# Kernel tuning notes

Measured on AMD Instinct MI355X. Metric: run time of the kernel, lower is better.

The kernel has to match this reference:

```python
import jax, jax.numpy as jnp
import numpy as np

B, S, D, H, FF = 2, 2048, 1024, 16, 4096
DK = D // H
MAX_SEQ_LEN = 2048
THETA = 10000.0
EPS = 1e-5


def _linear_init(key, out_f, in_f):
    std = (2.0 / (in_f + out_f)) ** 0.5
    return std * jax.random.truncated_normal(key, -3.0, 3.0, (out_f, in_f), dtype=jnp.float32)


def setup_inputs() -> dict:
    key = jax.random.key(0)
    ks = jax.random.split(key, 9)
    x = jax.random.normal(ks[0], (B, S, D), dtype=jnp.float32)
    token_positions = jnp.broadcast_to(jnp.arange(S, dtype=jnp.int32)[None, :], (B, S))
    return {
        "x": x,
        "wq": _linear_init(ks[1], D, D),
        "wk": _linear_init(ks[2], D, D),
        "wv": _linear_init(ks[3], D, D),
        "wo": _linear_init(ks[4], D, D),
        "w1": _linear_init(ks[5], FF, D),
        "w2": _linear_init(ks[6], D, FF),
        "w3": _linear_init(ks[7], FF, D),
        "g1": jnp.ones((D,), dtype=jnp.float32),
        "g2": jnp.ones((D,), dtype=jnp.float32),
        "token_positions": token_positions,
    }


def _rmsnorm(x, g):
    x32 = x.astype(jnp.float32)
    ms = jnp.sqrt(jnp.mean(x32 * x32, axis=-1, keepdims=True) + EPS)
    return ((x32 / ms) * g).astype(x.dtype)


def _rope(x, pos):
    # x: (B, H, S, DK); pos: (B, S)
    inv_freq = 1.0 / THETA ** (jnp.arange(0, DK, 2, dtype=jnp.float32) / DK)  # (DK/2,)
    freqs = pos.astype(jnp.float32)[..., None] * inv_freq  # (B, S, DK/2)
    cos = jnp.cos(freqs)[:, None, :, :]  # (B, 1, S, DK/2) broadcast over heads
    sin = jnp.sin(freqs)[:, None, :, :]
    x_real = x[..., 0::2]
    x_imag = x[..., 1::2]
    rot_real = x_real * cos - x_imag * sin
    rot_imag = x_real * sin + x_imag * cos
    return jnp.stack([rot_real, rot_imag], axis=-1).reshape(x.shape)


def reference(x, wq, wk, wv, wo, w1, w2, w3, g1, g2, token_positions):
    # --- attention sublayer ---
    h = _rmsnorm(x, g1)
    def proj(w):
        y = jnp.einsum('bsd,ed->bse', h, w)
        return y.reshape(B, S, H, DK).transpose(0, 2, 1, 3)  # (B,H,S,DK)
    Q = _rope(proj(wq), token_positions)
    K = _rope(proj(wk), token_positions)
    V = proj(wv)
    scores = jnp.einsum('bhqd,bhkd->bhqk', Q, K)  # (B,H,S,S) full matrix (naive)
    causal = jnp.tril(jnp.ones((S, S), dtype=bool))
    scores = jnp.where(causal, scores, -jnp.inf) / (DK ** 0.5)
    probs = jax.nn.softmax(scores, axis=-1)
    attn = jnp.einsum('bhqk,bhkd->bhqd', probs, V)
    attn = attn.transpose(0, 2, 1, 3).reshape(B, S, D)
    attn = jnp.einsum('bsd,ed->bse', attn, wo)
    y = x + attn
    # --- SwiGLU FFN sublayer ---
    h2 = _rmsnorm(y, g2)
    a = jnp.einsum('bsd,fd->bsf', h2, w1)
    gate = jnp.einsum('bsd,fd->bsf', h2, w3)
    ff = jnp.einsum('bsf,df->bsd', a * jax.nn.sigmoid(a) * gate, w2)
    return y + ff
```

## Files before the change

kernel.cpp:

```cpp
#include <hip/hip_runtime.h>
#include <hip/hip_bf16.h>

#define B_ 2
#define S_ 2048
#define D_ 1024
#define H_ 16
#define DK_ 64
#define FF_ 4096
#define M_ (B_ * S_)

typedef unsigned short u16;
typedef __bf16 bf16x8 __attribute__((ext_vector_type(8)));
typedef float f32x4 __attribute__((ext_vector_type(4)));
typedef u16 u16x4 __attribute__((ext_vector_type(4)));
typedef u16 u16x8 __attribute__((ext_vector_type(8)));

__device__ __forceinline__ u16 f2bf(float f) {
  __bf16 b = (__bf16)f;
  return __builtin_bit_cast(u16, b);
}
__device__ __forceinline__ float bf2f(u16 u) {
  __bf16 b = __builtin_bit_cast(__bf16, u);
  return (float)b;
}

__device__ __forceinline__ void async_lds16(const void* g, void* l) {
  __builtin_amdgcn_global_load_lds(
      (const __attribute__((address_space(1))) unsigned int*)g,
      (__attribute__((address_space(3))) unsigned int*)l, 16, 0, 0);
}

__device__ __forceinline__ void raw_barrier() {
  asm volatile("s_barrier" ::: "memory");
}
#define VMCNT_WAIT(n) asm volatile("s_waitcnt vmcnt(" #n ")" ::: "memory")

__global__ __launch_bounds__(256) void f2b_all(
    const float* __restrict__ wq, const float* __restrict__ wk,
    const float* __restrict__ wv, const float* __restrict__ wo,
    const float* __restrict__ w1, const float* __restrict__ w2,
    const float* __restrict__ w3, u16* __restrict__ wqkvb,
    u16* __restrict__ wob, u16* __restrict__ wb13, u16* __restrict__ w2b) {
  int i4 = blockIdx.x * 256 + threadIdx.x;
  const float* src;
  u16* dst;
  int off, oo;
  if (i4 < 262144) { src = wq; dst = wqkvb; off = i4; oo = off; }
  else if (i4 < 524288) { src = wk; dst = wqkvb + 1048576; off = i4 - 262144; oo = off; }
  else if (i4 < 786432) { src = wv; dst = wqkvb + 2097152; off = i4 - 524288; oo = off; }
  else if (i4 < 1048576) { src = wo; dst = wob; off = i4 - 786432; oo = off; }
  else if (i4 < 2097152) {
    src = w1; dst = wb13; off = i4 - 1048576;
    const int r = off >> 8;
    oo = (((r >> 4) * 32) + (r & 15)) * 256 + (off & 255);
  } else if (i4 < 3145728) { src = w2; dst = w2b; off = i4 - 2097152; oo = off; }
  else {
    src = w3; dst = wb13; off = i4 - 3145728;
    const int r = off >> 8;
    oo = (((r >> 4) * 32) + 16 + (r & 15)) * 256 + (off & 255);
  }
  float4 v = ((const float4*)src)[off];
  u16x4 o;
  o[0] = f2bf(v.x); o[1] = f2bf(v.y); o[2] = f2bf(v.z); o[3] = f2bf(v.w);
  *(u16x4*)(dst + (size_t)oo * 4) = o;
}

__global__ __launch_bounds__(256) void rmsnorm_k(const float* __restrict__ X,
                                                 const float* __restrict__ G,
                                                 u16* __restrict__ Out) {
  const int row = blockIdx.x, tid = threadIdx.x;
  const float4 xv = *(const float4*)(X + (size_t)row * D_ + tid * 4);
  float ss = xv.x * xv.x + xv.y * xv.y + xv.z * xv.z + xv.w * xv.w;
#pragma unroll
  for (int off = 1; off < 64; off <<= 1) ss += __shfl_xor(ss, off);
  __shared__ float red[4];
  if ((tid & 63) == 0) red[tid >> 6] = ss;
  __syncthreads();
  const float tot = red[0] + red[1] + red[2] + red[3];
  const float sc = rsqrtf(tot * (1.0f / D_) + 1e-5f);
  const float4 gv = *(const float4*)(G + tid * 4);
  u16x4 o;
  o[0] = f2bf(xv.x * sc * gv.x);
  o[1] = f2bf(xv.y * sc * gv.y);
  o[2] = f2bf(xv.z * sc * gv.z);
  o[3] = f2bf(xv.w * sc * gv.w);
  *(u16x4*)(Out + (size_t)row * D_ + tid * 4) = o;
}

__global__ __launch_bounds__(256) void rope2_k(unsigned int* __restrict__ Qb,
                                               unsigned int* __restrict__ Kb,
                                               const int* __restrict__ pos) {
  int idx = blockIdx.x * 256 + threadIdx.x;
  unsigned int* buf = Qb;
  float scale = 0.125f;
  if (idx >= 2097152) { buf = Kb; scale = 1.f; idx -= 2097152; }
  const int row = idx >> 9, p = idx & 511;
  const int i = p & 31;
  unsigned int v = buf[(size_t)row * 512 + p];
  const float xr = bf2f((u16)(v & 0xffffu));
  const float xi = bf2f((u16)(v >> 16));
  const float ang =
      (float)pos[row] * __expf(-(float)i * (9.210340371976184f / 32.0f));
  float sn, cs;
  sincosf(ang, &sn, &cs);
  const float orr = (xr * cs - xi * sn) * scale;
  const float oii = (xr * sn + xi * cs) * scale;
  buf[(size_t)row * 512 + p] =
      (unsigned int)f2bf(orr) | ((unsigned int)f2bf(oii) << 16);
}

__global__ __launch_bounds__(256) void transpose_v(const u16* __restrict__ V,
                                                   u16* __restrict__ Vt) {
  __shared__ __align__(16) u16 tile[32][64];
  const int tid = threadIdx.x;
  const int s0 = blockIdx.x * 32, bh = blockIdx.y, b = bh >> 4, h = bh & 15;
  {
    const int sr = tid >> 3, c = tid & 7;
    *(u16x8*)&tile[sr][c * 8] =
        *(const u16x8*)(V + (size_t)(b * S_ + s0 + sr) * D_ + h * DK_ + c * 8);
  }
  __syncthreads();
  {
    const int dk = tid >> 2, cs = tid & 3;
    u16x8 vv;
#pragma unroll
    for (int j = 0; j < 8; ++j) vv[j] = tile[cs * 8 + j][dk];
    *(u16x8*)(Vt + (size_t)(bh * DK_ + dk) * S_ + s0 + cs * 8) = vv;
  }
}

template <int RGN, int RGM>
__device__ __forceinline__ void region_map(int id, int gx, int BM, int BN,
                                           int& m0, int& n0) {
  const int xcd = id & 7, j = id >> 3;
  const int rcols = gx / RGN;
  m0 = ((xcd / rcols) * RGM + j / RGN) * BM;
  n0 = ((xcd % rcols) * RGN + (j % RGN)) * BN;
}

template <int EPI, int BN, int RGN, int RGM>
__global__ __launch_bounds__(512) void gemm8ph(const u16* __restrict__ A,
                                               const u16* __restrict__ Bw,
                                               void* __restrict__ Cout,
                                               const void* __restrict__ auxp,
                                               int N, int K) {
  constexpr int BM = 256, BK = 64;
  constexpr int CPR = BK / 8;
  constexpr int ACH = BM * CPR;
  constexpr int TCH = (BM + BN) * CPR;
  constexpr int NL = TCH / 512;
  constexpr int NR = BN / 64;
  __shared__ __align__(16) u16 As[2][BM * BK];
  __shared__ __align__(16) u16 Bs[2][BN * BK];
  const int tid = threadIdx.x, l = tid & 63, w = tid >> 6;
  const int gx = gridDim.x;
  const int id = blockIdx.y * gx + blockIdx.x;
  int m0, n0;
  region_map<RGN, RGM>(id, gx, BM, BN, m0, n0);
  const int wm = (w >> 2) * 128, wn = (w & 3) * (BN / 4);
  const int lr = l & 15, lg = l >> 4;

  f32x4 acc[8][NR] = {};

  auto STAGE_ALL = [&](int bf, int k0) {
#pragma unroll
    for (int i = 0; i < NL; ++i) {
      const int s = i * 512 + tid;
      const int base = i * 512 + w * 64;
      if (base < ACH) {
        const int r = s / CPR, ch = s % CPR;
        async_lds16(A + (size_t)(m0 + r) * K + k0 + ((ch ^ (r & 7)) * 8),
                    (char*)As[bf] + base * 16);
      } else {
        const int s2 = s - ACH;
        const int r = s2 / CPR, ch = s2 % CPR;
        async_lds16(Bw + (size_t)(n0 + r) * K + k0 + ((ch ^ (r & 7)) * 8),
                    (char*)Bs[bf] + (base - ACH) * 16);
      }
    }
  };

  STAGE_ALL(0, 0);
  VMCNT_WAIT(0);
  raw_barrier();
  int cur = 0;
  for (int k0 = 0; k0 < K; k0 += BK) {
    const bool more = (k0 + BK) < K;
    bf16x8 bfr[NR];
#pragma unroll
    for (int ph = 0; ph < 4; ++ph) {
      const int kk = ph >> 1, iq = ph & 1;
      if (iq == 0) {
#pragma unroll
        for (int j = 0; j < NR; ++j) {
          const int row = wn + j * 16 + lr;
          bfr[j] = *(const bf16x8*)&Bs[cur][row * BK +
                                            (((kk * 4 + lg) ^ (row & 7)) * 8)];
        }
      }
      bf16x8 af[4];
#pragma unroll
      for (int i = 0; i < 4; ++i) {
        const int row = wm + (iq * 4 + i) * 16 + lr;
        af[i] = *(const bf16x8*)&As[cur][row * BK +
                                         (((kk * 4 + lg) ^ (row & 7)) * 8)];
      }
      if (more && ph == 0) STAGE_ALL(cur ^ 1, k0 + BK);
      raw_barrier();
      __builtin_amdgcn_s_setprio(1);
#pragma unroll
      for (int i = 0; i < 4; ++i)
#pragma unroll
        for (int j = 0; j < NR; ++j)
          acc[iq * 4 + i][j] = __builtin_amdgcn_mfma_f32_16x16x32_bf16(
              af[i], bfr[j], acc[iq * 4 + i][j], 0, 0, 0);
      __builtin_amdgcn_s_setprio(0);
      if (ph < 3) raw_barrier();
    }
    if (more) {
      VMCNT_WAIT(0);
      raw_barrier();
    }
    cur ^= 1;
  }

#pragma unroll
  for (int i = 0; i < 8; ++i) {
#pragma unroll
    for (int j = 0; j < NR; ++j) {
#pragma unroll
      for (int t = 0; t < 4; ++t) {
        const int grow = m0 + wm + i * 16 + lg * 4 + t;
        const int gcol = n0 + wn + j * 16 + lr;
        const float v = acc[i][j][t];
        if (EPI == 0) {
          ((u16*)Cout)[(size_t)grow * N + gcol] = f2bf(v);
        } else if (EPI == 3) {
          u16* base = (u16*)Cout + (size_t)(gcol >> 10) * ((size_t)M_ * D_);
          base[(size_t)grow * D_ + (gcol & 1023)] = f2bf(v);
        } else if (EPI == 4) {
          if (j & 1) continue;
          const float a = v, g = acc[i][j + 1][t];
          const float sw = a / (1.f + __expf(-a)) * g;
          const int ocol = ((n0 + wn) >> 1) + (j >> 1) * 16 + lr;
          ((u16*)Cout)[(size_t)grow * FF_ + ocol] = f2bf(sw);
        }
      }
    }
  }
}

template <int BM, int BN, int BK, int EPI, int RGN, int RGM>
__global__ __launch_bounds__(512) void gemm2ph(const u16* __restrict__ A,
                                               const u16* __restrict__ Bw,
                                               void* __restrict__ Cout,
                                               const void* __restrict__ auxp,
                                               int N, int K) {
  constexpr int CPR = BK / 8;
  constexpr int ACH = BM * CPR;
  constexpr int TCH = (BM + BN) * CPR;
  constexpr int MR = BM / 32, NR = BN / 64;
  static_assert(TCH / 512 == 8, "vmcnt(8) assumes 8 loads/thread per STAGE");
  __shared__ __align__(16) u16 As[2][BM * BK];
  __shared__ __align__(16) u16 Bs[2][BN * BK];
  const int tid = threadIdx.x, l = tid & 63, w = tid >> 6;
  const int gx = gridDim.x;
  const int id = blockIdx.y * gx + blockIdx.x;
  int m0, n0;
  region_map<RGN, RGM>(id, gx, BM, BN, m0, n0);
  const int wm = (w >> 2) * (BM / 2), wn = (w & 3) * (BN / 4);
  const int lr = l & 15, lg = l >> 4;

  f32x4 acc[MR][NR] = {};

  auto STAGE = [&](int bf, int k0) {
#pragma unroll
    for (int i = 0; i < TCH / 512; ++i) {
      const int s = i * 512 + tid;
      const int base = i * 512 + w * 64;
      if (base < ACH) {
        const int r = s / CPR, ch = s % CPR;
        async_lds16(A + (size_t)(m0 + r) * K + k0 + ((ch ^ (r & 7)) * 8),
                    (char*)As[bf] + base * 16);
      } else {
        const int s2 = s - ACH;
        const int r = s2 / CPR, ch = s2 % CPR;
        async_lds16(Bw + (size_t)(n0 + r) * K + k0 + ((ch ^ (r & 7)) * 8),
                    (char*)Bs[bf] + (base - ACH) * 16);
      }
    }
  };

  STAGE(0, 0);
  int cur = 0;
  for (int k0 = 0; k0 < K; k0 += BK) {
    if (k0 + BK < K) {
      STAGE(cur ^ 1, k0 + BK);
      VMCNT_WAIT(8);
    } else {
      VMCNT_WAIT(0);
    }
    raw_barrier();
#pragma unroll
    for (int kk = 0; kk < BK / 32; ++kk) {
      bf16x8 af[MR], bfr[NR];
#pragma unroll
      for (int i = 0; i < MR; ++i) {
        const int row = wm + i * 16 + lr;
        af[i] = *(const bf16x8*)&As[cur][row * BK +
                                         (((kk * 4 + lg) ^ (row & 7)) * 8)];
      }
#pragma unroll
      for (int j = 0; j < NR; ++j) {
        const int row = wn + j * 16 + lr;
        bfr[j] = *(const bf16x8*)&Bs[cur][row * BK +
                                          (((kk * 4 + lg) ^ (row & 7)) * 8)];
      }
      __builtin_amdgcn_s_setprio(1);
#pragma unroll
      for (int i = 0; i < MR; ++i)
#pragma unroll
        for (int j = 0; j < NR; ++j)
          acc[i][j] = __builtin_amdgcn_mfma_f32_16x16x32_bf16(
              af[i], bfr[j], acc[i][j], 0, 0, 0);
      __builtin_amdgcn_s_setprio(0);
    }
    raw_barrier();
    cur ^= 1;
  }

#pragma unroll
  for (int i = 0; i < MR; ++i) {
#pragma unroll
    for (int j = 0; j < NR; ++j) {
#pragma unroll
      for (int t = 0; t < 4; ++t) {
        const int grow = m0 + wm + i * 16 + lg * 4 + t;
        const int gcol = n0 + wn + j * 16 + lr;
        const float v = acc[i][j][t];
        if (EPI == 0) {
          ((u16*)Cout)[(size_t)grow * N + gcol] = f2bf(v);
        } else if (EPI == 1) {
          const size_t idx = (size_t)grow * N + gcol;
          ((float*)Cout)[idx] = ((const float*)auxp)[idx] + v;
        }
      }
    }
  }
}

__global__ __launch_bounds__(256) void attn_fwd(const u16* __restrict__ Q,
                                                const u16* __restrict__ K,
                                                const u16* __restrict__ Vt,
                                                u16* __restrict__ O) {
  __shared__ __align__(16) u16 Ks[2][64 * 64];
  __shared__ __align__(16) u16 Vs[2][64 * 64];
  __shared__ __align__(16) u16 Ps[4][16 * 64];
  const int tid = threadIdx.x, l = tid & 63, w = tid >> 6;
  const int lr = l & 15, lg = l >> 4;
  const int bid = blockIdx.x;
  const int xcd = bid & 7, i = bid >> 3;
  const int bh = xcd * 4 + (i >> 5);
  const int qx = 31 - (i & 31);
  const int b = bh >> 4, h = bh & 15;
  const int q0w = qx * 64 + w * 16;

  const u16* Kb = K + (size_t)(b * S_) * D_ + h * DK_;
  const u16* Vb = Vt + (size_t)bh * DK_ * S_;

  bf16x8 aq[2];
  {
    const u16* qp = Q + (size_t)(b * S_ + q0w + lr) * D_ + h * DK_ + lg * 8;
    aq[0] = *(const bf16x8*)qp;
    aq[1] = *(const bf16x8*)(qp + 32);
  }
  f32x4 oacc[4] = {};
  float mrow[4], lrow[4];
#pragma unroll
  for (int t = 0; t < 4; ++t) { mrow[t] = -1e30f; lrow[t] = 0.f; }

  u16x8 ones_u;
#pragma unroll
  for (int j = 0; j < 8; ++j) ones_u[j] = 0x3F80;
  const bf16x8 ones = __builtin_bit_cast(bf16x8, ones_u);

  const int ntiles = qx + 1;

  auto STAGE = [&](int bf, int t) {
#pragma unroll
    for (int inst = 0; inst < 2; ++inst) {
      const int s = (w * 2 + inst) * 64 + l;
      const int r = s >> 3, ch = s & 7;
      const int chs = ch ^ (r & 7);
      async_lds16(Kb + (size_t)(t * 64 + r) * D_ + chs * 8,
                  (char*)Ks[bf] + (w * 2 + inst) * 1024);
      async_lds16(Vb + (size_t)r * S_ + t * 64 + chs * 8,
                  (char*)Vs[bf] + (w * 2 + inst) * 1024);
    }
  };

  auto PSTORE = [&](int r, int c, u16 v) {
    Ps[w][r * 64 + (c ^ ((r & 7) * 8))] = v;
  };

  STAGE(0, 0);
  int cur = 0;
  for (int it = 0; it < ntiles; ++it) {
    if (it + 1 < ntiles) {
      STAGE(cur ^ 1, it + 1);
      VMCNT_WAIT(4);
    } else {
      VMCNT_WAIT(0);
    }
    raw_barrier();
    f32x4 sf[4];
    __builtin_amdgcn_s_setprio(1);
#pragma unroll
    for (int n = 0; n < 4; ++n) {
      const int kvr = n * 16 + lr;
      f32x4 z = {};
      bf16x8 bk0 = *(const bf16x8*)&Ks[cur][kvr * 64 + ((lg ^ (kvr & 7)) * 8)];
      bf16x8 bk1 =
          *(const bf16x8*)&Ks[cur][kvr * 64 + (((4 + lg) ^ (kvr & 7)) * 8)];
      z = __builtin_amdgcn_mfma_f32_16x16x32_bf16(aq[0], bk0, z, 0, 0, 0);
      z = __builtin_amdgcn_mfma_f32_16x16x32_bf16(aq[1], bk1, z, 0, 0, 0);
      sf[n] = z;
    }
    __builtin_amdgcn_s_setprio(0);
    if (it < qx) {
      float fm[4];
      bool exc = false;
#pragma unroll
      for (int t = 0; t < 4; ++t) {
        fm[t] = fmaxf(fmaxf(sf[0][t], sf[1][t]), fmaxf(sf[2][t], sf[3][t]));
        exc |= fm[t] > mrow[t] + 8.f;
      }
      if (__any(exc)) {
#pragma unroll
        for (int t = 0; t < 4; ++t) {
          float mx = fm[t];
#pragma unroll
          for (int off = 1; off < 16; off <<= 1)
            mx = fmaxf(mx, __shfl_xor(mx, off));
          const float nm = fmaxf(mrow[t], mx);
          const float c = __expf(mrow[t] - nm);
          mrow[t] = nm;
          lrow[t] *= c;
#pragma unroll
          for (int d = 0; d < 4; ++d) oacc[d][t] *= c;
        }
      }
#pragma unroll
      for (int t = 0; t < 4; ++t)
#pragma unroll
        for (int n = 0; n < 4; ++n)
          PSTORE(lg * 4 + t, n * 16 + lr, f2bf(__expf(sf[n][t] - mrow[t])));
    } else {
      const int kv0 = it * 64;
#pragma unroll
      for (int t = 0; t < 4; ++t) {
        const int qrow = q0w + lg * 4 + t;
        float v[4];
#pragma unroll
        for (int n = 0; n < 4; ++n)
          v[n] = (kv0 + n * 16 + lr <= qrow) ? sf[n][t] : -1e30f;
        float mx = fmaxf(fmaxf(v[0], v[1]), fmaxf(v[2], v[3]));
#pragma unroll
        for (int off = 1; off < 16; off <<= 1)
          mx = fmaxf(mx, __shfl_xor(mx, off));
        const float nm = fmaxf(mrow[t], mx);
        const float c = __expf(mrow[t] - nm);
        mrow[t] = nm;
        lrow[t] *= c;
#pragma unroll
        for (int d = 0; d < 4; ++d) oacc[d][t] *= c;
#pragma unroll
        for (int n = 0; n < 4; ++n)
          PSTORE(lg * 4 + t, n * 16 + lr, f2bf(__expf(v[n] - nm)));
      }
    }
    bf16x8 ap0 = *(const bf16x8*)&Ps[w][lr * 64 + ((lg ^ (lr & 7)) * 8)];
    bf16x8 ap1 =
        *(const bf16x8*)&Ps[w][lr * 64 + (((4 + lg) ^ (lr & 7)) * 8)];
    __builtin_amdgcn_s_setprio(1);
    f32x4 zs = {};
    zs = __builtin_amdgcn_mfma_f32_16x16x32_bf16(ap0, ones, zs, 0, 0, 0);
    zs = __builtin_amdgcn_mfma_f32_16x16x32_bf16(ap1, ones, zs, 0, 0, 0);
#pragma unroll
    for (int d = 0; d < 4; ++d) {
      const int row = d * 16 + lr;
      bf16x8 bv0 = *(const bf16x8*)&Vs[cur][row * 64 + ((lg ^ (row & 7)) * 8)];
      bf16x8 bv1 =
          *(const bf16x8*)&Vs[cur][row * 64 + (((4 + lg) ^ (row & 7)) * 8)];
      oacc[d] = __builtin_amdgcn_mfma_f32_16x16x32_bf16(ap0, bv0, oacc[d], 0, 0, 0);
      oacc[d] = __builtin_amdgcn_mfma_f32_16x16x32_bf16(ap1, bv1, oacc[d], 0, 0, 0);
    }
    __builtin_amdgcn_s_setprio(0);
#pragma unroll
    for (int t = 0; t < 4; ++t) lrow[t] += zs[t];
    raw_barrier();
    cur ^= 1;
  }
#pragma unroll
  for (int d = 0; d < 4; ++d) {
#pragma unroll
    for (int t = 0; t < 4; ++t) {
      const size_t idx =
          (size_t)(b * S_ + q0w + lg * 4 + t) * D_ + h * DK_ + d * 16 + lr;
      O[idx] = f2bf(oacc[d][t] / lrow[t]);
    }
  }
}

extern "C" void kernel_launch(void* const* d_in, const int* in_sizes, int n_in,
                              void* d_out, int out_size, void* d_ws,
                              size_t ws_size, hipStream_t stream) {
  (void)in_sizes; (void)n_in; (void)out_size; (void)ws_size;
  const float* x = (const float*)d_in[0];
  const float* wq = (const float*)d_in[1];
  const float* wk = (const float*)d_in[2];
  const float* wv = (const float*)d_in[3];
  const float* wo = (const float*)d_in[4];
  const float* w1 = (const float*)d_in[5];
  const float* w2 = (const float*)d_in[6];
  const float* w3 = (const float*)d_in[7];
  const float* g1 = (const float*)d_in[8];
  const float* g2 = (const float*)d_in[9];
  const int* tp = (const int*)d_in[10];
  float* out = (float*)d_out;

  char* ws = (char*)d_ws;
  const size_t MB = 1024u * 1024u;
  u16* wqkvb = (u16*)(ws + 0 * MB);
  u16* wob  = (u16*)(ws + 6 * MB);
  u16* wb13 = (u16*)(ws + 8 * MB);
  u16* w2b  = (u16*)(ws + 24 * MB);
  u16* hb   = (u16*)(ws + 32 * MB);
  float* yb = (float*)(ws + 40 * MB);
  u16* h2b  = (u16*)(ws + 56 * MB);
  u16* Qb   = (u16*)(ws + 64 * MB);
  u16* Kb   = (u16*)(ws + 72 * MB);
  u16* Vb   = (u16*)(ws + 80 * MB);
  u16* Vtb  = (u16*)(ws + 88 * MB);
  u16* ffb  = (u16*)(ws + 96 * MB);
  u16* aob  = hb;

  f2b_all<<<16384, 256, 0, stream>>>(wq, wk, wv, wo, w1, w2, w3, wqkvb, wob,
                                     wb13, w2b);

  rmsnorm_k<<<4096, 256, 0, stream>>>(x, g1, hb);

  gemm8ph<3, 192, 4, 8><<<dim3(16, 16), 512, 0, stream>>>(
      hb, wqkvb, Qb, nullptr, 3072, 1024);

  rope2_k<<<16384, 256, 0, stream>>>((unsigned int*)Qb, (unsigned int*)Kb, tp);
  transpose_v<<<dim3(64, 32), 256, 0, stream>>>(Vb, Vtb);

  attn_fwd<<<1024, 256, 0, stream>>>(Qb, Kb, Vtb, aob);

  gemm2ph<128, 128, 128, 1, 4, 8><<<dim3(8, 32), 512, 0, stream>>>(
      aob, wob, yb, x, 1024, 1024);
  rmsnorm_k<<<4096, 256, 0, stream>>>(yb, g2, h2b);

  gemm8ph<4, 256, 8, 8><<<dim3(32, 16), 512, 0, stream>>>(
      h2b, wb13, ffb, nullptr, 8192, 1024);
  gemm2ph<128, 128, 128, 1, 4, 8><<<dim3(8, 32), 512, 0, stream>>>(
      ffb, w2b, out, yb, 1024, 4096);
}
```

Measured before the change: 279.8 us.

## Fuse RoPE and V transpose into the QKV GEMM epilogue

The QKV projection GEMM epilogue now applies rotary embedding to the Q and K columns, pairing adjacent even and odd columns with a lane shuffle and folding the 1/sqrt(dk) scale into Q. It also writes V directly in transposed per-head layout. This removes the separate rope and transpose kernels and their extra global-memory round trips and launches. In exchange the epilogue does more work, computing sin/cos with fast intrinsics (__sinf/__cosf) that can lose accuracy at large angles, and the transposed V stores are strided 8-byte writes.

```diff
diff --git a/kernel.cpp b/kernel.cpp
--- a/kernel.cpp
+++ b/kernel.cpp
@@ -87,48 +87,6 @@
   *(u16x4*)(Out + (size_t)row * D_ + tid * 4) = o;
 }
 
-__global__ __launch_bounds__(256) void rope2_k(unsigned int* __restrict__ Qb,
-                                               unsigned int* __restrict__ Kb,
-                                               const int* __restrict__ pos) {
-  int idx = blockIdx.x * 256 + threadIdx.x;
-  unsigned int* buf = Qb;
-  float scale = 0.125f;
-  if (idx >= 2097152) { buf = Kb; scale = 1.f; idx -= 2097152; }
-  const int row = idx >> 9, p = idx & 511;
-  const int i = p & 31;
-  unsigned int v = buf[(size_t)row * 512 + p];
-  const float xr = bf2f((u16)(v & 0xffffu));
-  const float xi = bf2f((u16)(v >> 16));
-  const float ang =
-      (float)pos[row] * __expf(-(float)i * (9.210340371976184f / 32.0f));
-  float sn, cs;
-  sincosf(ang, &sn, &cs);
-  const float orr = (xr * cs - xi * sn) * scale;
-  const float oii = (xr * sn + xi * cs) * scale;
-  buf[(size_t)row * 512 + p] =
-      (unsigned int)f2bf(orr) | ((unsigned int)f2bf(oii) << 16);
-}
-
-__global__ __launch_bounds__(256) void transpose_v(const u16* __restrict__ V,
-                                                   u16* __restrict__ Vt) {
-  __shared__ __align__(16) u16 tile[32][64];
-  const int tid = threadIdx.x;
-  const int s0 = blockIdx.x * 32, bh = blockIdx.y, b = bh >> 4, h = bh & 15;
-  {
-    const int sr = tid >> 3, c = tid & 7;
-    *(u16x8*)&tile[sr][c * 8] =
-        *(const u16x8*)(V + (size_t)(b * S_ + s0 + sr) * D_ + h * DK_ + c * 8);
-  }
-  __syncthreads();
-  {
-    const int dk = tid >> 2, cs = tid & 3;
-    u16x8 vv;
-#pragma unroll
-    for (int j = 0; j < 8; ++j) vv[j] = tile[cs * 8 + j][dk];
-    *(u16x8*)(Vt + (size_t)(bh * DK_ + dk) * S_ + s0 + cs * 8) = vv;
-  }
-}
-
 template <int RGN, int RGM>
 __device__ __forceinline__ void region_map(int id, int gx, int BM, int BN,
                                            int& m0, int& n0) {
@@ -143,7 +101,8 @@
                                                const u16* __restrict__ Bw,
                                                void* __restrict__ Cout,
                                                const void* __restrict__ auxp,
-                                               int N, int K) {
+                                               int N, int K,
+                                               const int* __restrict__ tp) {
   constexpr int BM = 256, BK = 64;
   constexpr int CPR = BK / 8;
   constexpr int ACH = BM * CPR;
@@ -224,26 +183,64 @@
     cur ^= 1;
   }
 
-#pragma unroll
-  for (int i = 0; i < 8; ++i) {
-#pragma unroll
-    for (int j = 0; j < NR; ++j) {
-#pragma unroll
-      for (int t = 0; t < 4; ++t) {
-        const int grow = m0 + wm + i * 16 + lg * 4 + t;
+  if (EPI == 0 || EPI == 4) {
+#pragma unroll
+    for (int i = 0; i < 8; ++i) {
+#pragma unroll
+      for (int j = 0; j < NR; ++j) {
+#pragma unroll
+        for (int t = 0; t < 4; ++t) {
+          const int grow = m0 + wm + i * 16 + lg * 4 + t;
+          const int gcol = n0 + wn + j * 16 + lr;
+          const float v = acc[i][j][t];
+          if (EPI == 0) {
+            ((u16*)Cout)[(size_t)grow * N + gcol] = f2bf(v);
+          } else {
+            if (j & 1) continue;
+            const float a = v, g = acc[i][j + 1][t];
+            const float sw = a / (1.f + __expf(-a)) * g;
+            const int ocol = ((n0 + wn) >> 1) + (j >> 1) * 16 + lr;
+            ((u16*)Cout)[(size_t)grow * FF_ + ocol] = f2bf(sw);
+          }
+        }
+      }
+    }
+  } else {
+#pragma unroll
+    for (int i = 0; i < 8; ++i) {
+      const int grow0 = m0 + wm + i * 16 + lg * 4;
+      float posf[4];
+#pragma unroll
+      for (int t = 0; t < 4; ++t) posf[t] = (float)tp[grow0 + t];
+      const int bb = grow0 >> 11, s0 = grow0 & 2047;
+#pragma unroll
+      for (int j = 0; j < NR; ++j) {
         const int gcol = n0 + wn + j * 16 + lr;
-        const float v = acc[i][j][t];
-        if (EPI == 0) {
-          ((u16*)Cout)[(size_t)grow * N + gcol] = f2bf(v);
-        } else if (EPI == 3) {
-          u16* base = (u16*)Cout + (size_t)(gcol >> 10) * ((size_t)M_ * D_);
-          base[(size_t)grow * D_ + (gcol & 1023)] = f2bf(v);
-        } else if (EPI == 4) {
-          if (j & 1) continue;
-          const float a = v, g = acc[i][j + 1][t];
-          const float sw = a / (1.f + __expf(-a)) * g;
-          const int ocol = ((n0 + wn) >> 1) + (j >> 1) * 16 + lr;
-          ((u16*)Cout)[(size_t)grow * FF_ + ocol] = f2bf(sw);
+        const int region = gcol >> 10;
+        if (region < 2) {
+          u16* dst = (u16*)Cout + (size_t)region * ((size_t)M_ * D_);
+          const float qscale = (region == 0) ? 0.125f : 1.0f;
+          const float invf = __expf(-(float)((gcol & 63) >> 1) *
+                                    (9.210340371976184f / 32.0f));
+          const float sgn = (gcol & 1) ? 1.f : -1.f;
+#pragma unroll
+          for (int t = 0; t < 4; ++t) {
+            const float own = acc[i][j][t];
+            const float pe = __shfl_xor(own, 1);
+            const float ang = posf[t] * invf;
+            const float sn = __sinf(ang), cs = __cosf(ang);
+            dst[(size_t)(grow0 + t) * D_ + (gcol & 1023)] =
+                f2bf((own * cs + sgn * pe * sn) * qscale);
+          }
+        } else {
+          u16* vt = (u16*)Cout + 2 * ((size_t)M_ * D_);
+          const int vcol = gcol & 1023;
+          u16x4 pk;
+#pragma unroll
+          for (int t = 0; t < 4; ++t) pk[t] = f2bf(acc[i][j][t]);
+          const size_t addr =
+              ((size_t)(bb * 16 + (vcol >> 6)) * 64 + (vcol & 63)) * 2048 + s0;
+          *(u16x4*)(vt + addr) = pk;
         }
       }
     }
@@ -540,8 +537,7 @@
   u16* h2b  = (u16*)(ws + 56 * MB);
   u16* Qb   = (u16*)(ws + 64 * MB);
   u16* Kb   = (u16*)(ws + 72 * MB);
-  u16* Vb   = (u16*)(ws + 80 * MB);
-  u16* Vtb  = (u16*)(ws + 88 * MB);
+  u16* Vtb  = (u16*)(ws + 80 * MB);
   u16* ffb  = (u16*)(ws + 96 * MB);
   u16* aob  = hb;
 
@@ -551,10 +547,7 @@
   rmsnorm_k<<<4096, 256, 0, stream>>>(x, g1, hb);
 
   gemm8ph<3, 192, 4, 8><<<dim3(16, 16), 512, 0, stream>>>(
-      hb, wqkvb, Qb, nullptr, 3072, 1024);
-
-  rope2_k<<<16384, 256, 0, stream>>>((unsigned int*)Qb, (unsigned int*)Kb, tp);
-  transpose_v<<<dim3(64, 32), 256, 0, stream>>>(Vb, Vtb);
+      hb, wqkvb, Qb, nullptr, 3072, 1024, tp);
 
   attn_fwd<<<1024, 256, 0, stream>>>(Qb, Kb, Vtb, aob);
 
@@ -563,7 +556,7 @@
   rmsnorm_k<<<4096, 256, 0, stream>>>(yb, g2, h2b);
 
   gemm8ph<4, 256, 8, 8><<<dim3(32, 16), 512, 0, stream>>>(
-      h2b, wb13, ffb, nullptr, 8192, 1024);
+      h2b, wb13, ffb, nullptr, 8192, 1024, nullptr);
   gemm2ph<128, 128, 128, 1, 4, 8><<<dim3(8, 32), 512, 0, stream>>>(
       ffb, w2b, out, yb, 1024, 4096);
 }
```

Measured after the change: 271.1 us (median of 2 runs). 3.1% less time.
